# Kernel tuning notes

Hardware: AMD Instinct MI355X
Metric: run time of the kernel (lower is better)

## Reference

```python
import jax, jax.numpy as jnp
import numpy as np

B = 8192      # batch
E = 16        # n_experts
D = 128       # per-expert input dim (equal for all experts)
U = 256       # units
F = 256       # feature_dim (gating input)
G = 4         # n_gates
K = 6         # hard-coded top-k in the original call()
TEMP = 0.01   # hard-coded softmax temperature
LEAKY_SLOPE = 0.2  # keras leaky_relu default negative slope


def setup_inputs() -> dict:
    key = jax.random.key(0)
    ks = jax.random.split(key, 5)
    return {
        "inputs": jax.random.normal(ks[0], (B, E * D), dtype=jnp.float32),
        "feature_input": jax.random.normal(ks[1], (B, F), dtype=jnp.float32),
        # stacked per-expert kernels (equal dims -> one [E, D, U] tensor)
        "expert_kernels": jax.random.normal(ks[2], (E, D, U), dtype=jnp.float32) * 0.05,
        "expert_biases": jnp.zeros((E, U), dtype=jnp.float32),
        "gating_kernels": jax.random.normal(ks[3], (G, F, E), dtype=jnp.float32) * 0.1,
        "gating_biases": jnp.zeros((G, E), dtype=jnp.float32),
        "global_weights": jnp.ones((E,), dtype=jnp.float32),
    }


def reference(inputs, feature_input, expert_kernels, expert_biases,
              gating_kernels, gating_biases, global_weights):
    # ---- per-expert dense + bias + LeakyReLU (tf.split loop -> batched einsum) ----
    x = inputs.reshape(B, E, D)                                   # [B, E, D]
    eo = jnp.einsum('bed,edu->bue', x, expert_kernels)            # [B, U, E]
    eo = eo + expert_biases.T[None, :, :]                         # bias per expert
    expert_outputs = jax.nn.leaky_relu(eo, LEAKY_SLOPE)           # [B, U, E]

    # ---- gating: dense + bias + ReLU, scaled by global_weights ----
    g = jnp.einsum('bf,gfe->bge', feature_input, gating_kernels)  # [B, G, E]
    g = jax.nn.relu(g + gating_biases[None, :, :]) * global_weights

    # sharp softmax over experts, then top-k selection
    p = jax.nn.softmax(g / TEMP, axis=-1)                         # [B, G, E]
    top_v, top_i = jax.lax.top_k(p, K)                            # [B, G, K]

    # gather selected expert outputs: [B, G, U, K]
    sel = jnp.take_along_axis(expert_outputs[:, None, :, :],
                              top_i[:, :, None, :], axis=-1)

    # renormalize top-k values with another sharp softmax, weighted combine
    w = jax.nn.softmax(top_v / TEMP, axis=-1)                     # [B, G, K]
    out = jnp.einsum('bguk,bgk->bgu', sel, w)                     # [B, G, U]
    concat_output = out.reshape(B, G * U)                         # concat over gates
    return concat_output, expert_outputs
```

## Files before the change

kernel.cpp:

```cpp
#include <hip/hip_runtime.h>
#include <stdint.h>

#define NB 8192
#define NE 16
#define ND 128
#define NU 256
#define NF 256
#define NG 4
#define NK 6
#define ITEMP_LOG2E 144.26950408889634f

typedef short short4v __attribute__((ext_vector_type(4)));
typedef short short8v __attribute__((ext_vector_type(8)));
typedef float float4v __attribute__((ext_vector_type(4)));

__device__ __forceinline__ short f2bf(float x) {
  uint32_t u = __builtin_bit_cast(uint32_t, x);
  u += 0x7FFFu + ((u >> 16) & 1u);
  return (short)(u >> 16);
}

__global__ __launch_bounds__(256) void prep_kernel(
    const float* __restrict__ ek,
    short* __restrict__ pb)
{
  int gid = (blockIdx.x << 8) | threadIdx.x;
  int lane = gid & 63, ut = (gid >> 6) & 15, ks = (gid >> 10) & 3, e = gid >> 12;
  int krow = ks * 32 + ((lane >> 4) * 8);
  int ucol = ut * 16 + (lane & 15);
  const float* src = ek + (size_t)(e * 128 + krow) * 256 + ucol;
  short8v v;
#pragma unroll
  for (int j = 0; j < 8; ++j) v[j] = f2bf(src[(size_t)j * 256]);
  size_t widx = (((size_t)ut * 16 + e) * 4 + ks) * 64 + lane;
  *(short8v*)(pb + widx * 8) = v;
}

#define APITCH 2056
#define WPITCH 64

__global__ __launch_bounds__(1024, 4) void moe_kernel(
    const float* __restrict__ x,
    const float* __restrict__ feat,
    const float* __restrict__ gk,
    const float* __restrict__ gbias,
    const float* __restrict__ gw,
    const float* __restrict__ eb,
    const short* __restrict__ pb,
    float* __restrict__ out)
{
  __shared__ __align__(16) short ash[32 * APITCH];
  __shared__ __align__(16) float wsh[32 * WPITCH];
  __shared__ __align__(16) float stg[16 * 256];
  int bt = blockIdx.x, tid = threadIdx.x;
  int w = tid >> 6, lane = tid & 63;

  if (w < 12) {
    const float4v* s = (const float4v*)(x + (size_t)bt * 32 * 2048);
    int base = w * 64 + lane;
    float4v buf[11];
#pragma unroll
    for (int k = 0; k < 11; ++k) buf[k] = __builtin_nontemporal_load(s + base + k * 768);
#pragma unroll
    for (int k = 0; k < 11; ++k) {
      int idx = base + k * 768;
      int row = idx >> 9, colf = (idx & 511) << 2;
      short4v sv;
      sv[0] = f2bf(buf[k][0]); sv[1] = f2bf(buf[k][1]);
      sv[2] = f2bf(buf[k][2]); sv[3] = f2bf(buf[k][3]);
      *(short4v*)&ash[row * APITCH + colf] = sv;
    }
#pragma unroll
    for (int k = 0; k < 10; ++k) buf[k] = __builtin_nontemporal_load(s + base + (11 + k) * 768);
#pragma unroll
    for (int k = 0; k < 10; ++k) {
      int idx = base + (11 + k) * 768;
      int row = idx >> 9, colf = (idx & 511) << 2;
      short4v sv;
      sv[0] = f2bf(buf[k][0]); sv[1] = f2bf(buf[k][1]);
      sv[2] = f2bf(buf[k][2]); sv[3] = f2bf(buf[k][3]);
      *(short4v*)&ash[row * APITCH + colf] = sv;
    }
    if (base < 256) {
      int idx = base + 16128;
      float4v v = __builtin_nontemporal_load(s + idx);
      int row = idx >> 9, colf = (idx & 511) << 2;
      short4v sv;
      sv[0] = f2bf(v[0]); sv[1] = f2bf(v[1]); sv[2] = f2bf(v[2]); sv[3] = f2bf(v[3]);
      *(short4v*)&ash[row * APITCH + colf] = sv;
    }
  } else {
    int rb = (w - 12) * 8;
    int gate = lane >> 4, e = lane & 15;
    float gwv = gw[e];
    float bias = gbias[gate * 16 + e];
    const float* gkp = gk + (size_t)gate * (NF * NE) + e;
    const float* fb = feat + ((size_t)bt * 32 + rb) * 256;
    float acc[8];
#pragma unroll
    for (int i = 0; i < 8; ++i) acc[i] = bias;
#pragma unroll 1
    for (int f0 = 0; f0 < NF; f0 += 16) {
      float gv[16];
#pragma unroll
      for (int j = 0; j < 16; ++j) gv[j] = gkp[(f0 + j) * 16];
#pragma unroll
      for (int j = 0; j < 16; j += 4) {
#pragma unroll
        for (int i = 0; i < 8; ++i) {
          float4v fv = *(const float4v*)(fb + i * 256 + f0 + j);
          acc[i] = fmaf(fv[0], gv[j + 0], acc[i]);
          acc[i] = fmaf(fv[1], gv[j + 1], acc[i]);
          acc[i] = fmaf(fv[2], gv[j + 2], acc[i]);
          acc[i] = fmaf(fv[3], gv[j + 3], acc[i]);
        }
      }
    }
#pragma unroll 1
    for (int i = 0; i < 8; ++i) {
      float v = acc[i] > 0.f ? acc[i] : 0.f;
      v *= gwv;
      float m = v;
#pragma unroll
      for (int off = 1; off < 16; off <<= 1) m = fmaxf(m, __shfl_xor(m, off, 16));
      float ex = exp2f((v - m) * ITEMP_LOG2E);
      float s = ex;
#pragma unroll
      for (int off = 1; off < 16; off <<= 1) s += __shfl_xor(s, off, 16);
      float pr = ex / s;
      float cur = pr;
      float topv[NK]; int topi[NK];
#pragma unroll
      for (int r = 0; r < NK; ++r) {
        float mv = cur;
#pragma unroll
        for (int off = 1; off < 16; off <<= 1) mv = fmaxf(mv, __shfl_xor(mv, off, 16));
        int cand = (cur == mv) ? e : 16;
#pragma unroll
        for (int off = 1; off < 16; off <<= 1) cand = min(cand, __shfl_xor(cand, off, 16));
        topv[r] = mv; topi[r] = cand;
        if (e == cand) cur = -1.f;
      }
      float wv[NK], wsum = 0.f;
#pragma unroll
      for (int r = 0; r < NK; ++r) {
        wv[r] = exp2f((topv[r] - topv[0]) * ITEMP_LOG2E);
        wsum += wv[r];
      }
      float inv = 1.f / wsum;
      float wdv = 0.f;
#pragma unroll
      for (int r = 0; r < NK; ++r) wdv = (topi[r] == e) ? wv[r] * inv : wdv;
      wsh[(rb + i) * WPITCH + lane] = wdv;
    }
  }
  __syncthreads();

  int btile = w >> 3, utq = (w >> 1) & 3, th = w & 1;
  int q = lane >> 4, col = lane & 15;
  int am = lane & 15;
  float* outcat = out;
  float* outeo = out + (size_t)NB * NG * NU;
  const short8v* pbv = (const short8v*)pb;
  float* ws = stg + w * 256;
  size_t bb = (size_t)bt * 32 + btile * 16;
  int arow = (btile * 16 + am) * APITCH;
  int wrow = (btile * 16 + q * 4) * WPITCH;

  float csave[4][4];

#pragma unroll 1
  for (int tl = 0; tl < 2; ++tl) {
    int t = th * 2 + tl;
    int ut = utq * 4 + t;
    const short8v* bp = pbv + (size_t)ut * 4096;
    float4v acc[16];
    float4v zero = {0.f, 0.f, 0.f, 0.f};
#pragma unroll
    for (int e = 0; e < 16; ++e) acc[e] = zero;
    short8v bA[4], bB[4];
#pragma unroll
    for (int ks = 0; ks < 4; ++ks) bA[ks] = bp[ks * 64 + lane];
#pragma unroll
    for (int e = 0; e < 16; e += 2) {
#pragma unroll
      for (int ks = 0; ks < 4; ++ks) bB[ks] = bp[(e + 1) * 256 + ks * 64 + lane];
#pragma unroll
      for (int ks = 0; ks < 4; ++ks) {
        short8v a = *(const short8v*)&ash[arow + e * 128 + ks * 32 + q * 8];
        acc[e] = __builtin_amdgcn_mfma_f32_16x16x32_bf16(a, bA[ks], acc[e], 0, 0, 0);
      }
      if (e + 2 < 16) {
#pragma unroll
        for (int ks = 0; ks < 4; ++ks) bA[ks] = bp[(e + 2) * 256 + ks * 64 + lane];
      }
#pragma unroll
      for (int ks = 0; ks < 4; ++ks) {
        short8v a = *(const short8v*)&ash[arow + (e + 1) * 128 + ks * 32 + q * 8];
        acc[e + 1] = __builtin_amdgcn_mfma_f32_16x16x32_bf16(a, bB[ks], acc[e + 1], 0, 0, 0);
      }
    }
    float v[16][4];
#pragma unroll
    for (int e = 0; e < 16; ++e) {
      float bv = eb[e * 256 + ut * 16 + col];
#pragma unroll
      for (int r = 0; r < 4; ++r) {
        float z = acc[e][r] + bv;
        v[e][r] = z > 0.f ? z : 0.2f * z;
      }
    }
#pragma unroll
    for (int r = 0; r < 4; ++r) {
#pragma unroll
      for (int qq = 0; qq < 4; ++qq) {
        if (q == qq) {
#pragma unroll
          for (int c = 0; c < 4; ++c) {
            float4v o = {v[4 * c + 0][r], v[4 * c + 1][r], v[4 * c + 2][r], v[4 * c + 3][r]};
            *(float4v*)(ws + (c * 16 + col) * 4) = o;
          }
        }
        __builtin_amdgcn_wave_barrier();
        {
          size_t b = bb + (size_t)(qq * 4 + r);
          float4v val = *(const float4v*)(ws + lane * 4);
          float* dst = outeo + b * 4096 + (size_t)ut * 256 + (lane & 15) * 16 + (lane >> 4) * 4;
          *(float4v*)dst = val;
        }
        __builtin_amdgcn_wave_barrier();
      }
    }
#pragma unroll
    for (int r = 0; r < 4; ++r) {
      size_t b = bb + (size_t)(q * 4 + r);
#pragma unroll
      for (int g = 0; g < 4; ++g) {
        float sacc = 0.f;
#pragma unroll
        for (int ec = 0; ec < 16; ec += 4) {
          float4v wv = *(const float4v*)&wsh[wrow + r * WPITCH + g * 16 + ec];
          sacc = fmaf(wv[0], v[ec][r], sacc);
          sacc = fmaf(wv[1], v[ec + 1][r], sacc);
          sacc = fmaf(wv[2], v[ec + 2][r], sacc);
          sacc = fmaf(wv[3], v[ec + 3][r], sacc);
        }
        if (tl == 0) {
          csave[r][g] = sacc;
        } else {
          float* cb = outcat + b * 1024 + g * 256 + (ut - 1) * 16 + col;
          cb[0] = csave[r][g];
          cb[16] = sacc;
        }
      }
    }
  }
}

extern "C" void kernel_launch(void* const* d_in, const int* in_sizes, int n_in,
                              void* d_out, int out_size, void* d_ws, size_t ws_size,
                              hipStream_t stream) {
  const float* x     = (const float*)d_in[0];
  const float* feat  = (const float*)d_in[1];
  const float* ek    = (const float*)d_in[2];
  const float* eb    = (const float*)d_in[3];
  const float* gk    = (const float*)d_in[4];
  const float* gbias = (const float*)d_in[5];
  const float* gw    = (const float*)d_in[6];
  float* out = (float*)d_out;
  short* pbf = (short*)d_ws;

  prep_kernel<<<256, 256, 0, stream>>>(ek, pbf);
  moe_kernel<<<256, 1024, 0, stream>>>(x, feat, gk, gbias, gw, eb, pbf, out);
}
```

Measured before the change: 327.0 us.

## Split fused MoE kernel into gating/prep, expert GEMM, and combine kernels

Moves the gating computation into the weight-prep kernel, which writes per-row gate weights to workspace. The expert GEMM becomes its own kernel with 16-row tiles and 512 threads, giving more blocks and less shared memory per block. The weighted combine becomes a separate pass that re-reads the expert outputs from global memory. This aims to free the GEMM from idle gating waves and raise occupancy, at the cost of an extra round trip of the 128MB expert output tensor and an added launch.

```diff
diff --git a/kernel.cpp b/kernel.cpp
--- a/kernel.cpp
+++ b/kernel.cpp
@@ -22,80 +22,34 @@
 
 __global__ __launch_bounds__(256) void prep_kernel(
     const float* __restrict__ ek,
-    short* __restrict__ pb)
-{
-  int gid = (blockIdx.x << 8) | threadIdx.x;
-  int lane = gid & 63, ut = (gid >> 6) & 15, ks = (gid >> 10) & 3, e = gid >> 12;
-  int krow = ks * 32 + ((lane >> 4) * 8);
-  int ucol = ut * 16 + (lane & 15);
-  const float* src = ek + (size_t)(e * 128 + krow) * 256 + ucol;
-  short8v v;
-#pragma unroll
-  for (int j = 0; j < 8; ++j) v[j] = f2bf(src[(size_t)j * 256]);
-  size_t widx = (((size_t)ut * 16 + e) * 4 + ks) * 64 + lane;
-  *(short8v*)(pb + widx * 8) = v;
-}
-
-#define APITCH 2056
-#define WPITCH 64
-
-__global__ __launch_bounds__(1024, 4) void moe_kernel(
-    const float* __restrict__ x,
     const float* __restrict__ feat,
     const float* __restrict__ gk,
     const float* __restrict__ gbias,
     const float* __restrict__ gw,
-    const float* __restrict__ eb,
-    const short* __restrict__ pb,
-    float* __restrict__ out)
+    short* __restrict__ pb,
+    float* __restrict__ wd)
 {
-  __shared__ __align__(16) short ash[32 * APITCH];
-  __shared__ __align__(16) float wsh[32 * WPITCH];
-  __shared__ __align__(16) float stg[16 * 256];
-  int bt = blockIdx.x, tid = threadIdx.x;
-  int w = tid >> 6, lane = tid & 63;
-
-  if (w < 12) {
-    const float4v* s = (const float4v*)(x + (size_t)bt * 32 * 2048);
-    int base = w * 64 + lane;
-    float4v buf[11];
-#pragma unroll
-    for (int k = 0; k < 11; ++k) buf[k] = __builtin_nontemporal_load(s + base + k * 768);
-#pragma unroll
-    for (int k = 0; k < 11; ++k) {
-      int idx = base + k * 768;
-      int row = idx >> 9, colf = (idx & 511) << 2;
-      short4v sv;
-      sv[0] = f2bf(buf[k][0]); sv[1] = f2bf(buf[k][1]);
-      sv[2] = f2bf(buf[k][2]); sv[3] = f2bf(buf[k][3]);
-      *(short4v*)&ash[row * APITCH + colf] = sv;
-    }
-#pragma unroll
-    for (int k = 0; k < 10; ++k) buf[k] = __builtin_nontemporal_load(s + base + (11 + k) * 768);
-#pragma unroll
-    for (int k = 0; k < 10; ++k) {
-      int idx = base + (11 + k) * 768;
-      int row = idx >> 9, colf = (idx & 511) << 2;
-      short4v sv;
-      sv[0] = f2bf(buf[k][0]); sv[1] = f2bf(buf[k][1]);
-      sv[2] = f2bf(buf[k][2]); sv[3] = f2bf(buf[k][3]);
-      *(short4v*)&ash[row * APITCH + colf] = sv;
-    }
-    if (base < 256) {
-      int idx = base + 16128;
-      float4v v = __builtin_nontemporal_load(s + idx);
-      int row = idx >> 9, colf = (idx & 511) << 2;
-      short4v sv;
-      sv[0] = f2bf(v[0]); sv[1] = f2bf(v[1]); sv[2] = f2bf(v[2]); sv[3] = f2bf(v[3]);
-      *(short4v*)&ash[row * APITCH + colf] = sv;
-    }
+  int bid = blockIdx.x, tid = threadIdx.x;
+  if (bid < 256) {
+    int gid = (bid << 8) | tid;
+    int lane = gid & 63, ut = (gid >> 6) & 15, ks = (gid >> 10) & 3, e = gid >> 12;
+    int krow = ks * 32 + ((lane >> 4) * 8);
+    int ucol = ut * 16 + (lane & 15);
+    const float* src = ek + (size_t)(e * 128 + krow) * 256 + ucol;
+    short8v v;
+#pragma unroll
+    for (int j = 0; j < 8; ++j) v[j] = f2bf(src[(size_t)j * 256]);
+    size_t widx = (((size_t)ut * 16 + e) * 4 + ks) * 64 + lane;
+    *(short8v*)(pb + widx * 8) = v;
   } else {
-    int rb = (w - 12) * 8;
+    int w = tid >> 6, lane = tid & 63;
+    int rb = w * 8;
     int gate = lane >> 4, e = lane & 15;
     float gwv = gw[e];
     float bias = gbias[gate * 16 + e];
     const float* gkp = gk + (size_t)gate * (NF * NE) + e;
-    const float* fb = feat + ((size_t)bt * 32 + rb) * 256;
+    size_t b0 = (size_t)(bid - 256) * 32 + rb;
+    const float* fb = feat + b0 * 256;
     float acc[8];
 #pragma unroll
     for (int i = 0; i < 8; ++i) acc[i] = bias;
@@ -151,28 +105,56 @@
       float wdv = 0.f;
 #pragma unroll
       for (int r = 0; r < NK; ++r) wdv = (topi[r] == e) ? wv[r] * inv : wdv;
-      wsh[(rb + i) * WPITCH + lane] = wdv;
+      wd[(b0 + i) * 64 + lane] = wdv;
+    }
+  }
+}
+
+#define APITCH 2056
+
+__global__ __launch_bounds__(512, 4) void gemm_kernel(
+    const float* __restrict__ x,
+    const float* __restrict__ eb,
+    const short* __restrict__ pb,
+    float* __restrict__ outeo)
+{
+  __shared__ __align__(16) short ash[16 * APITCH];
+  __shared__ __align__(16) float stg[8 * 256];
+  int bt = blockIdx.x, tid = threadIdx.x;
+  int w = tid >> 6, lane = tid & 63;
+
+  {
+    const float4v* s = (const float4v*)(x + (size_t)bt * 16 * 2048);
+    float4v buf[8];
+#pragma unroll
+    for (int c = 0; c < 2; ++c) {
+#pragma unroll
+      for (int k = 0; k < 8; ++k)
+        buf[k] = __builtin_nontemporal_load(s + tid + (c * 8 + k) * 512);
+#pragma unroll
+      for (int k = 0; k < 8; ++k) {
+        int idx = tid + (c * 8 + k) * 512;
+        int row = idx >> 9, colf = (idx & 511) << 2;
+        short4v sv;
+        sv[0] = f2bf(buf[k][0]); sv[1] = f2bf(buf[k][1]);
+        sv[2] = f2bf(buf[k][2]); sv[3] = f2bf(buf[k][3]);
+        *(short4v*)&ash[row * APITCH + colf] = sv;
+      }
     }
   }
   __syncthreads();
 
-  int btile = w >> 3, utq = (w >> 1) & 3, th = w & 1;
+  int utq = w & 3, th = w >> 2;
   int q = lane >> 4, col = lane & 15;
   int am = lane & 15;
-  float* outcat = out;
-  float* outeo = out + (size_t)NB * NG * NU;
   const short8v* pbv = (const short8v*)pb;
   float* ws = stg + w * 256;
-  size_t bb = (size_t)bt * 32 + btile * 16;
-  int arow = (btile * 16 + am) * APITCH;
-  int wrow = (btile * 16 + q * 4) * WPITCH;
-
-  float csave[4][4];
+  size_t bb = (size_t)bt * 16;
+  int arow = am * APITCH;
 
 #pragma unroll 1
   for (int tl = 0; tl < 2; ++tl) {
-    int t = th * 2 + tl;
-    int ut = utq * 4 + t;
+    int ut = utq * 4 + th * 2 + tl;
     const short8v* bp = pbv + (size_t)ut * 4096;
     float4v acc[16];
     float4v zero = {0.f, 0.f, 0.f, 0.f};
@@ -231,28 +213,37 @@
         __builtin_amdgcn_wave_barrier();
       }
     }
-#pragma unroll
-    for (int r = 0; r < 4; ++r) {
-      size_t b = bb + (size_t)(q * 4 + r);
-#pragma unroll
-      for (int g = 0; g < 4; ++g) {
-        float sacc = 0.f;
-#pragma unroll
-        for (int ec = 0; ec < 16; ec += 4) {
-          float4v wv = *(const float4v*)&wsh[wrow + r * WPITCH + g * 16 + ec];
-          sacc = fmaf(wv[0], v[ec][r], sacc);
-          sacc = fmaf(wv[1], v[ec + 1][r], sacc);
-          sacc = fmaf(wv[2], v[ec + 2][r], sacc);
-          sacc = fmaf(wv[3], v[ec + 3][r], sacc);
-        }
-        if (tl == 0) {
-          csave[r][g] = sacc;
-        } else {
-          float* cb = outcat + b * 1024 + g * 256 + (ut - 1) * 16 + col;
-          cb[0] = csave[r][g];
-          cb[16] = sacc;
-        }
-      }
+  }
+}
+
+__global__ __launch_bounds__(256) void combine_kernel(
+    const float* __restrict__ eo,
+    const float* __restrict__ wd,
+    float* __restrict__ outcat)
+{
+  __shared__ float wl[256];
+  int bt = blockIdx.x, tid = threadIdx.x;
+  wl[tid] = wd[(size_t)bt * 256 + tid];
+  __syncthreads();
+#pragma unroll 1
+  for (int i = 0; i < 4; ++i) {
+    size_t b = (size_t)bt * 4 + i;
+    const float4v* ep = (const float4v*)(eo + b * 4096 + (size_t)tid * 16);
+    float4v e0 = ep[0], e1 = ep[1], e2 = ep[2], e3 = ep[3];
+    const float* wp = wl + i * 64;
+#pragma unroll
+    for (int g = 0; g < 4; ++g) {
+      const float* wg = wp + g * 16;
+      float s = 0.f;
+      s = fmaf(wg[0],  e0[0], s); s = fmaf(wg[1],  e0[1], s);
+      s = fmaf(wg[2],  e0[2], s); s = fmaf(wg[3],  e0[3], s);
+      s = fmaf(wg[4],  e1[0], s); s = fmaf(wg[5],  e1[1], s);
+      s = fmaf(wg[6],  e1[2], s); s = fmaf(wg[7],  e1[3], s);
+      s = fmaf(wg[8],  e2[0], s); s = fmaf(wg[9],  e2[1], s);
+      s = fmaf(wg[10], e2[2], s); s = fmaf(wg[11], e2[3], s);
+      s = fmaf(wg[12], e3[0], s); s = fmaf(wg[13], e3[1], s);
+      s = fmaf(wg[14], e3[2], s); s = fmaf(wg[15], e3[3], s);
+      outcat[b * 1024 + g * 256 + tid] = s;
     }
   }
 }
@@ -268,8 +259,12 @@
   const float* gbias = (const float*)d_in[5];
   const float* gw    = (const float*)d_in[6];
   float* out = (float*)d_out;
-  short* pbf = (short*)d_ws;
-
-  prep_kernel<<<256, 256, 0, stream>>>(ek, pbf);
-  moe_kernel<<<256, 1024, 0, stream>>>(x, feat, gk, gbias, gw, eb, pbf, out);
-}
+  float* outcat = out;
+  float* outeo  = out + (size_t)NB * NG * NU;
+  float* wd  = (float*)d_ws;
+  short* pbf = (short*)((char*)d_ws + (size_t)NB * NG * NE * 4);
+
+  prep_kernel<<<512, 256, 0, stream>>>(ek, feat, gk, gbias, gw, pbf, wd);
+  gemm_kernel<<<512, 512, 0, stream>>>(x, eb, pbf, outeo);
+  combine_kernel<<<2048, 256, 0, stream>>>(outeo, wd, outcat);
+}
```

Result: no change. 323.0 us (-1.2%).
